# Optimization experiments

Measured on AMD Instinct MI355X. Metric: run time of the kernel, lower is better.

## Reference

```python
import jax, jax.numpy as jnp
import numpy as np
import math

SCALES = (1, 2, 4)
GROUPS = 8
EPS = 1e-5
TEMPERATURE = 1.0


def bilinear_resize(x, out_h, out_w):
    # torch F.interpolate mode='bilinear', align_corners=False
    B, C, h, w = x.shape
    def coords(out, in_):
        c = (jnp.arange(out, dtype=x.dtype) + 0.5) * (in_ / out) - 0.5
        c = jnp.clip(c, 0.0, in_ - 1.0)
        i0 = jnp.floor(c).astype(jnp.int32)
        i1 = jnp.minimum(i0 + 1, in_ - 1)
        t = c - i0.astype(x.dtype)
        return i0, i1, t
    y0, y1, ty = coords(out_h, h)
    x0, x1, tx = coords(out_w, w)
    r0 = x[:, :, y0, :]
    r1 = x[:, :, y1, :]
    v00 = r0[:, :, :, x0]; v01 = r0[:, :, :, x1]
    v10 = r1[:, :, :, x0]; v11 = r1[:, :, :, x1]
    top = v00 * (1.0 - tx) + v01 * tx
    bot = v10 * (1.0 - tx) + v11 * tx
    return top * (1.0 - ty)[:, None] + bot * ty[:, None]


def group_norm(x, gamma, beta):
    B, C, H, W = x.shape
    xg = x.reshape(B, GROUPS, C // GROUPS, H, W)
    mu = xg.mean(axis=(2, 3, 4), keepdims=True)
    var = xg.var(axis=(2, 3, 4), keepdims=True)
    xn = ((xg - mu) * jax.lax.rsqrt(var + EPS)).reshape(B, C, H, W)
    return xn * gamma[None, :, None, None] + beta[None, :, None, None]


def setup_inputs() -> dict:
    key = jax.random.key(0)
    B, C, H, W = 4, 128, 64, 64
    inter = max(C // 4, 8)  # 32
    S = len(SCALES)
    ks = jax.random.split(key, 8)
    def xavier(k, shape, fan_in, fan_out):
        a = math.sqrt(6.0 / (fan_in + fan_out))
        return jax.random.uniform(k, shape, jnp.float32, -a, a)
    inp = {
        'x': jax.random.normal(ks[0], (B, C, H, W), jnp.float32),
        'gn_w': jnp.ones((S, C), jnp.float32),
        'gn_b': jnp.zeros((S, C), jnp.float32),
        'qw': xavier(ks[1], (S, inter, C), C, inter),
        'qb': jnp.zeros((S, inter), jnp.float32),
        'kw': xavier(ks[2], (S, inter, C), C, inter),
        'kb': jnp.zeros((S, inter), jnp.float32),
        'vw': xavier(ks[3], (S, inter, C), C, inter),
        'vb': jnp.zeros((S, inter), jnp.float32),
        'ow': xavier(ks[4], (S, C, inter), inter, C),
        'ob': jnp.zeros((S, C), jnp.float32),
        'gamma': jnp.full((S,), 0.1 / S, jnp.float32),
        'scale_weights': jnp.full((S,), 1.0 / S, jnp.float32),
    }
    return inp


def _forward(x, gn_w, gn_b, qw, qb, kw, kb, vw, vb, ow, ob, gamma, scale_weights):
    B, C, H, W = x.shape
    inter = qw.shape[1]
    inv_scale = 1.0 / (TEMPERATURE * math.sqrt(inter))
    outs = []
    for i, s in enumerate(SCALES):
        if s == 1:
            xs = x
        else:
            xs = x.reshape(B, C, H // s, s, W // s, s).mean(axis=(3, 5))
        h, w = xs.shape[2], xs.shape[3]
        N = h * w
        xn = group_norm(xs, gn_w[i], gn_b[i])
        # 1x1 convs as channel contractions
        q = (jnp.einsum('oc,bchw->bohw', qw[i], xn) + qb[i][None, :, None, None]).reshape(B, inter, N)
        k = (jnp.einsum('oc,bchw->bohw', kw[i], xn) + kb[i][None, :, None, None]).reshape(B, inter, N)
        v = (jnp.einsum('oc,bchw->bohw', vw[i], xn) + vb[i][None, :, None, None]).reshape(B, inter, N)
        logits = jnp.einsum('bin,bim->bnm', q, k) * inv_scale  # [B, N, N]
        attn = jax.nn.softmax(logits, axis=-1)
        att = jnp.einsum('bnm,bim->bin', attn, v).reshape(B, inter, h, w)
        o = jnp.einsum('ci,bihw->bchw', ow[i], att) + ob[i][None, :, None, None]
        y = gamma[i] * o + xs
        if s > 1:
            y = bilinear_resize(y, H, W)
        outs.append(y)
    wts = jax.nn.softmax(scale_weights, axis=0)
    fused = wts[0] * outs[0]
    for i in range(1, len(outs)):
        fused = fused + wts[i] * outs[i]
    return fused


def reference(x, gn_w, gn_b, qw, qb, kw, kb, vw, vb, ow, ob, gamma, scale_weights):
    return _forward(x, gn_w, gn_b, qw, qb, kw, kb, vw, vb, ow, ob, gamma, scale_weights)
```

## Files before the change

kernel.cpp:

```cpp
#include <hip/hip_runtime.h>
#include <math.h>

#define B 4
#define C 128
#define G 8
#define CPG 16
#define INTER 32
#define SPLIT 16
#define KS 4

#define N1 4096
#define N2 1024
#define N4 256

#define QOFF2 (B * N1 * 32)
#define QOFF4 (QOFF2 + B * N2 * 32)
#define QTOT  (QOFF4 + B * N4 * 32)
#define PAOFF2 (B * KS * 32 * N1)
#define PAOFF4 (PAOFF2 + B * KS * 32 * N2)
#define PATOT  (PAOFF4 + B * KS * 32 * N4)
#define PMOFF2 (B * KS * 2 * N1)
#define PMOFF4 (PMOFF2 + B * KS * 2 * N2)
#define PMTOT  (PMOFF4 + B * KS * 2 * N4)

typedef unsigned short ushort_t;
typedef __attribute__((ext_vector_type(8))) short short8;
typedef __attribute__((ext_vector_type(4))) short short4v;
typedef __attribute__((ext_vector_type(4))) float f32x4;

__device__ __forceinline__ ushort_t f2bf(float f) {
    union { float f; unsigned u; } x; x.f = f;
    unsigned r = x.u + 0x7fffu + ((x.u >> 16) & 1u);
    return (ushort_t)(r >> 16);
}

__device__ __forceinline__ void scale_wts(const float* __restrict__ sw,
                                          float& w0, float& w1, float& w2) {
    float a = sw[0], b = sw[1], c = sw[2];
    float m = fmaxf(a, fmaxf(b, c));
    float e0 = __expf(a - m), e1 = __expf(b - m), e2 = __expf(c - m);
    float inv = 1.0f / (e0 + e1 + e2);
    w0 = e0 * inv; w1 = e1 * inv; w2 = e2 * inv;
}

__device__ __forceinline__ void block_reduce_write(float s, float q,
                                                   float* __restrict__ dst2) {
    __shared__ float rs[256], rq[256];
    rs[threadIdx.x] = s; rq[threadIdx.x] = q;
    __syncthreads();
    for (int st = 128; st > 0; st >>= 1) {
        if (threadIdx.x < st) {
            rs[threadIdx.x] += rs[threadIdx.x + st];
            rq[threadIdx.x] += rq[threadIdx.x + st];
        }
        __syncthreads();
    }
    if (threadIdx.x == 0) { dst2[0] = rs[0]; dst2[1] = rq[0]; }
}

__global__ __launch_bounds__(256) void pool_stats_kernel(const float* __restrict__ x,
                                                         float* __restrict__ xs2,
                                                         float* __restrict__ xs4,
                                                         float* __restrict__ part) {
    int bid = blockIdx.x;
    if (bid < 512) {
        int sp = bid & 15, bg = bid >> 4;
        const float* base = x + ((bg * CPG) << 12) + sp * 4096;
        float s = 0.0f, q = 0.0f;
        for (int i = threadIdx.x; i < 4096; i += 256) {
            float v = base[i];
            s += v; q += v * v;
        }
        block_reduce_write(s, q, part + bid * 2);
    } else if (bid < 1024) {
        int blk = bid - 512;
        int sp = blk & 15, bg = blk >> 4;
        int bc = bg * CPG + sp;
        const float* src = x + (bc << 12);
        float* dst = xs2 + (bc << 10);
        float s = 0.0f, q = 0.0f;
        for (int p = threadIdx.x; p < 1024; p += 256) {
            int oy = p >> 5, ox = p & 31;
            const float* s2 = src + oy * 128 + ox * 2;
            float v = (s2[0] + s2[1] + s2[64] + s2[65]) * 0.25f;
            dst[p] = v; s += v; q += v * v;
        }
        block_reduce_write(s, q, part + 1024 + blk * 2);
    } else {
        int blk = bid - 1024;
        int sp = blk & 15, bg = blk >> 4;
        int bc = bg * CPG + sp;
        const float* src = x + (bc << 12);
        float* dst = xs4 + (bc << 8);
        float s = 0.0f, q = 0.0f;
        if (threadIdx.x < 256) {
            int p = threadIdx.x;
            int oy = p >> 4, ox = p & 15;
            const float* s4 = src + oy * 256 + ox * 4;
            float v = 0.0f;
            #pragma unroll
            for (int dy = 0; dy < 4; ++dy)
                #pragma unroll
                for (int dx = 0; dx < 4; ++dx) v += s4[dy * 64 + dx];
            v *= 0.0625f;
            dst[p] = v; s = v; q = v * v;
        }
        block_reduce_write(s, q, part + 2048 + blk * 2);
    }
}

template <int N, int NSH>
__device__ __forceinline__ void qkv_body(int bi, const float* __restrict__ xs,
    const float* __restrict__ part,
    const float* __restrict__ gn_w, const float* __restrict__ gn_b,
    const float* __restrict__ qw, const float* __restrict__ qb,
    const float* __restrict__ kw, const float* __restrict__ kb,
    const float* __restrict__ vw, const float* __restrict__ vb,
    ushort_t* __restrict__ q_bf, ushort_t* __restrict__ k_bf, ushort_t* __restrict__ v_bf) {
    const int nc = N >> 8;
    int nchunk = bi % nc; bi /= nc;
    int og = bi & 3; bi >>= 2;
    int proj = bi % 3; int b = bi / 3;
    const float* wp = (proj == 0) ? qw : ((proj == 1) ? kw : vw);
    const float* bp = (proj == 0) ? qb : ((proj == 1) ? kb : vb);
    __shared__ float wl[8 * 128];
    __shared__ float2 ss[128];
    {
        int t = threadIdx.x;
        #pragma unroll
        for (int r = 0; r < 4; ++r) {
            int e = r * 256 + t;
            int o = e >> 7, c0 = e & 127;
            wl[c0 * 8 + o] = wp[(og * 8 + o) * C + c0];
        }
        if (t < 128) {
            int c = t;
            int bg = b * 8 + (c >> 4);
            float s = 0.0f, q = 0.0f;
            #pragma unroll
            for (int sp = 0; sp < SPLIT; ++sp) {
                s += part[(bg * SPLIT + sp) * 2];
                q += part[(bg * SPLIT + sp) * 2 + 1];
            }
            float inv = 1.0f / (float)(CPG << NSH);
            float mu = s * inv;
            float var = q * inv - mu * mu;
            float rsig = rsqrtf(var + 1e-5f);
            float a = rsig * gn_w[c];
            float2 r; r.x = a; r.y = gn_b[c] - mu * a;
            ss[c] = r;
        }
    }
    __syncthreads();
    int n = nchunk * 256 + threadIdx.x;
    const float* xb = xs + ((size_t)(b * C) << NSH) + n;
    float acc[8];
    #pragma unroll
    for (int o = 0; o < 8; ++o) acc[o] = bp[og * 8 + o];
    #pragma unroll 2
    for (int c0 = 0; c0 < C; ++c0) {
        float raw = xb[(size_t)c0 << NSH];
        float2 s2 = ss[c0];
        float xv = fmaf(s2.x, raw, s2.y);
        const float4* wr = (const float4*)&wl[c0 * 8];
        float4 w0 = wr[0], w1 = wr[1];
        acc[0] += w0.x * xv; acc[1] += w0.y * xv; acc[2] += w0.z * xv; acc[3] += w0.w * xv;
        acc[4] += w1.x * xv; acc[5] += w1.y * xv; acc[6] += w1.z * xv; acc[7] += w1.w * xv;
    }
    if (proj < 2) {
        ushort_t tmp[8];
        #pragma unroll
        for (int o = 0; o < 8; ++o) tmp[o] = f2bf(acc[o]);
        ushort_t* dst = ((proj == 0) ? q_bf : k_bf) + ((size_t)(b * N + n)) * 32 + og * 8;
        *(uint4*)dst = *(const uint4*)tmp;
    } else {
        #pragma unroll
        for (int o = 0; o < 8; ++o)
            v_bf[((size_t)(b * 32 + og * 8 + o) << NSH) + n] = f2bf(acc[o]);
    }
}

__global__ __launch_bounds__(256) void qkv_all_kernel(const float* __restrict__ x,
    const float* __restrict__ xs2, const float* __restrict__ xs4,
    const float* __restrict__ part,
    const float* __restrict__ gn_w, const float* __restrict__ gn_b,
    const float* __restrict__ qw, const float* __restrict__ qb,
    const float* __restrict__ kw, const float* __restrict__ kb,
    const float* __restrict__ vw, const float* __restrict__ vb,
    ushort_t* __restrict__ qbf, ushort_t* __restrict__ kbf, ushort_t* __restrict__ vbf) {
    int bid = blockIdx.x;
    if (bid < 768) {
        qkv_body<N1, 12>(bid, x, part, gn_w, gn_b, qw, qb, kw, kb, vw, vb, qbf, kbf, vbf);
    } else if (bid < 960) {
        qkv_body<N2, 10>(bid - 768, xs2, part + 1024, gn_w + C, gn_b + C,
                         qw + INTER * C, qb + INTER, kw + INTER * C, kb + INTER,
                         vw + INTER * C, vb + INTER,
                         qbf + QOFF2, kbf + QOFF2, vbf + QOFF2);
    } else {
        qkv_body<N4, 8>(bid - 960, xs4, part + 2048, gn_w + 2 * C, gn_b + 2 * C,
                        qw + 2 * INTER * C, qb + 2 * INTER, kw + 2 * INTER * C, kb + 2 * INTER,
                        vw + 2 * INTER * C, vb + 2 * INTER,
                        qbf + QOFF4, kbf + QOFF4, vbf + QOFF4);
    }
}

template <int N, int NSH>
__device__ __forceinline__ void attn_body(int bi,
    const ushort_t* __restrict__ q_bf, const ushort_t* __restrict__ k_bf,
    const ushort_t* __restrict__ v_bf,
    float* __restrict__ pacc, float* __restrict__ pml,
    ushort_t* K_lds, ushort_t* V_lds, ushort_t* P_lds) {
    int ks = bi % KS; bi /= KS;
    const int nqc = N >> 6;
    int qc = bi % nqc; int b = bi / nqc;
    int tid = threadIdx.x;
    int l = tid & 63, w = tid >> 6, lq = l & 15, g = l >> 4;
    int q0 = qc * 64 + w * 16;
    const float invs = 0.17677669529663687f;

    short8 qf = *(const short8*)(q_bf + ((size_t)(b * N + q0 + lq)) * 32 + g * 8);
    f32x4 acco0 = {0.f, 0.f, 0.f, 0.f}, acco1 = {0.f, 0.f, 0.f, 0.f};
    float mrun = -3.0e38f, lrun = 0.0f;

    const int kchunk = N / KS;
    int kbase = ks * kchunk;
    const int ntiles = kchunk >> 6;
    ushort_t* Pw = P_lds + w * 16 * 72;

    for (int t = 0; t < ntiles; ++t) {
        int kt0 = kbase + t * 64;
        __syncthreads();
        {
            const uint4* ksrc = (const uint4*)(k_bf + ((size_t)(b * N + kt0 + (tid >> 2))) * 32 + (tid & 3) * 8);
            *(uint4*)&K_lds[(tid >> 2) * 40 + (tid & 3) * 8] = *ksrc;
            const uint4* vsrc = (const uint4*)(v_bf + (((size_t)(b * 32 + (tid >> 3))) << NSH) + kt0 + (tid & 7) * 8);
            *(uint4*)&V_lds[(tid >> 3) * 72 + (tid & 7) * 8] = *vsrc;
        }
        __syncthreads();

        f32x4 sa[4];
        #pragma unroll
        for (int kt = 0; kt < 4; ++kt) {
            short8 kf = *(const short8*)&K_lds[(kt * 16 + lq) * 40 + g * 8];
            f32x4 z = {0.f, 0.f, 0.f, 0.f};
            sa[kt] = __builtin_amdgcn_mfma_f32_16x16x32_bf16(kf, qf, z, 0, 0, 0);
        }
        float sc[16];
        #pragma unroll
        for (int kt = 0; kt < 4; ++kt) {
            sc[kt * 4 + 0] = sa[kt][0] * invs;
            sc[kt * 4 + 1] = sa[kt][1] * invs;
            sc[kt * 4 + 2] = sa[kt][2] * invs;
            sc[kt * 4 + 3] = sa[kt][3] * invs;
        }
        float tmax = sc[0];
        #pragma unroll
        for (int j = 1; j < 16; ++j) tmax = fmaxf(tmax, sc[j]);
        tmax = fmaxf(tmax, __shfl_xor(tmax, 16, 64));
        tmax = fmaxf(tmax, __shfl_xor(tmax, 32, 64));
        float nm = fmaxf(mrun, tmax);
        float corr = __expf(mrun - nm);
        float psum = 0.0f;
        ushort_t pb[16];
        #pragma unroll
        for (int j = 0; j < 16; ++j) {
            float p = __expf(sc[j] - nm);
            psum += p;
            pb[j] = f2bf(p);
        }
        psum += __shfl_xor(psum, 16, 64);
        psum += __shfl_xor(psum, 32, 64);
        lrun = lrun * corr + psum;
        mrun = nm;
        #pragma unroll
        for (int e = 0; e < 4; ++e) { acco0[e] *= corr; acco1[e] *= corr; }
        #pragma unroll
        for (int kt = 0; kt < 4; ++kt) {
            short4v pv4;
            pv4[0] = (short)pb[kt * 4 + 0];
            pv4[1] = (short)pb[kt * 4 + 1];
            pv4[2] = (short)pb[kt * 4 + 2];
            pv4[3] = (short)pb[kt * 4 + 3];
            *(short4v*)&Pw[lq * 72 + kt * 16 + g * 4] = pv4;
        }
        #pragma unroll
        for (int c = 0; c < 2; ++c) {
            short8 pf  = *(const short8*)&Pw[lq * 72 + c * 32 + g * 8];
            short8 vf0 = *(const short8*)&V_lds[(lq) * 72 + c * 32 + g * 8];
            short8 vf1 = *(const short8*)&V_lds[(16 + lq) * 72 + c * 32 + g * 8];
            acco0 = __builtin_amdgcn_mfma_f32_16x16x32_bf16(vf0, pf, acco0, 0, 0, 0);
            acco1 = __builtin_amdgcn_mfma_f32_16x16x32_bf16(vf1, pf, acco1, 0, 0, 0);
        }
    }
    int n = q0 + lq;
    size_t pb_ = ((size_t)(b * KS + ks)) * 32;
    #pragma unroll
    for (int r = 0; r < 4; ++r) {
        pacc[(pb_ + (g * 4 + r)) * N + n]      = acco0[r];
        pacc[(pb_ + 16 + (g * 4 + r)) * N + n] = acco1[r];
    }
    if (g == 0) {
        pml[((size_t)(b * KS + ks) * 2) * N + n]     = mrun;
        pml[((size_t)(b * KS + ks) * 2 + 1) * N + n] = lrun;
    }
}

__global__ __launch_bounds__(256) void attn_all_kernel(
    const ushort_t* __restrict__ qbf, const ushort_t* __restrict__ kbf,
    const ushort_t* __restrict__ vbf,
    float* __restrict__ pacc, float* __restrict__ pml) {
    __shared__ ushort_t K_lds[64 * 40];
    __shared__ ushort_t V_lds[32 * 72];
    __shared__ ushort_t P_lds[4 * 16 * 72];
    int bid = blockIdx.x;
    if (bid < 1024) {
        attn_body<N1, 12>(bid, qbf, kbf, vbf, pacc, pml, K_lds, V_lds, P_lds);
    } else if (bid < 1280) {
        attn_body<N2, 10>(bid - 1024, qbf + QOFF2, kbf + QOFF2, vbf + QOFF2,
                          pacc + PAOFF2, pml + PMOFF2, K_lds, V_lds, P_lds);
    } else {
        attn_body<N4, 8>(bid - 1280, qbf + QOFF4, kbf + QOFF4, vbf + QOFF4,
                         pacc + PAOFF4, pml + PMOFF4, K_lds, V_lds, P_lds);
    }
}

template <int N, int NSH>
__device__ __forceinline__ void comb_oy_body(int tile, const float* __restrict__ pacc,
                                             const float* __restrict__ pml,
                                             const float* __restrict__ ow,
                                             const float* __restrict__ ob,
                                             const float* __restrict__ gamma,
                                             const float* __restrict__ xs,
                                             float* __restrict__ ydst,
                                             const float* __restrict__ sw,
                                             float* att_lds, float* ow_lds) {
    const int ntiles = N >> 5;
    int b = tile / ntiles;
    int n0 = (tile % ntiles) << 5;
    int t = threadIdx.x;
    {
        const float4* src = (const float4*)ow;
        float4* dst = (float4*)ow_lds;
        dst[t] = src[t];
        dst[256 + t] = src[256 + t];
        dst[512 + t] = src[512 + t];
        dst[768 + t] = src[768 + t];
    }
    {
        int o = t >> 3, j = t & 3, half = (t >> 2) & 1;
        o = t >> 3; j = t & 7;
        int n = n0 + j * 4;
        float4 mv[KS], lv[KS], av[KS];
        float4 M = {-3.0e38f, -3.0e38f, -3.0e38f, -3.0e38f};
        #pragma unroll
        for (int ks = 0; ks < KS; ++ks) {
            mv[ks] = *(const float4*)&pml[((size_t)(b * KS + ks) * 2) * N + n];
            lv[ks] = *(const float4*)&pml[((size_t)(b * KS + ks) * 2 + 1) * N + n];
            av[ks] = *(const float4*)&pacc[((size_t)(b * KS + ks) * INTER + o) * N + n];
            M.x = fmaxf(M.x, mv[ks].x); M.y = fmaxf(M.y, mv[ks].y);
            M.z = fmaxf(M.z, mv[ks].z); M.w = fmaxf(M.w, mv[ks].w);
        }
        float4 L = {0.f, 0.f, 0.f, 0.f}, A = {0.f, 0.f, 0.f, 0.f};
        #pragma unroll
        for (int ks = 0; ks < KS; ++ks) {
            float4 wgt;
            wgt.x = __expf(mv[ks].x - M.x); wgt.y = __expf(mv[ks].y - M.y);
            wgt.z = __expf(mv[ks].z - M.z); wgt.w = __expf(mv[ks].w - M.w);
            L.x += lv[ks].x * wgt.x; L.y += lv[ks].y * wgt.y;
            L.z += lv[ks].z * wgt.z; L.w += lv[ks].w * wgt.w;
            A.x += av[ks].x * wgt.x; A.y += av[ks].y * wgt.y;
            A.z += av[ks].z * wgt.z; A.w += av[ks].w * wgt.w;
        }
        float4 r;
        r.x = A.x / L.x; r.y = A.y / L.y; r.z = A.z / L.z; r.w = A.w / L.w;
        *(float4*)&att_lds[o * 36 + j * 4] = r;
    }
    __syncthreads();
    {
        int n = t & 31;
        int cg = t >> 5;
        float av[INTER];
        #pragma unroll
        for (int i = 0; i < INTER; ++i) av[i] = att_lds[i * 36 + n];
        float gm = gamma[0];
        float wsc = 1.0f;
        bool scale = (sw != nullptr);
        if (scale) { float w0, w1, w2; scale_wts(sw, w0, w1, w2); wsc = w0; }
        const float* xsb = xs + ((size_t)(b * C + cg * 16) << NSH) + n0 + n;
        float* yb = ydst + ((size_t)(b * C + cg * 16) << NSH) + n0 + n;
        #pragma unroll
        for (int cc = 0; cc < 16; ++cc) {
            int c = cg * 16 + cc;
            const float4* wr = (const float4*)&ow_lds[c * 32];
            float a0 = 0.f, a1 = 0.f, a2 = 0.f, a3 = 0.f;
            #pragma unroll
            for (int i4 = 0; i4 < 8; ++i4) {
                float4 wv = wr[i4];
                a0 += wv.x * av[i4 * 4 + 0];
                a1 += wv.y * av[i4 * 4 + 1];
                a2 += wv.z * av[i4 * 4 + 2];
                a3 += wv.w * av[i4 * 4 + 3];
            }
            float o = ob[c] + ((a0 + a1) + (a2 + a3));
            float y = gm * o + xsb[(size_t)cc << NSH];
            yb[(size_t)cc << NSH] = wsc * y;
        }
    }
}

__global__ __launch_bounds__(256) void comb_oy_all_kernel(const float* __restrict__ pacc,
    const float* __restrict__ pml,
    const float* __restrict__ ow, const float* __restrict__ ob,
    const float* __restrict__ gamma,
    const float* __restrict__ x, const float* __restrict__ xs2, const float* __restrict__ xs4,
    float* __restrict__ out, float* __restrict__ y2, float* __restrict__ y4,
    const float* __restrict__ sw) {
    __shared__ float att_lds[32 * 36];
    __shared__ float ow_lds[128 * 32];
    int bid = blockIdx.x;
    if (bid < 512) {
        comb_oy_body<N1, 12>(bid, pacc, pml, ow, ob, gamma, x, out, sw, att_lds, ow_lds);
    } else if (bid < 640) {
        comb_oy_body<N2, 10>(bid - 512, pacc + PAOFF2, pml + PMOFF2,
                             ow + C * INTER, ob + C, gamma + 1, xs2, y2, nullptr,
                             att_lds, ow_lds);
    } else {
        comb_oy_body<N4, 8>(bid - 640, pacc + PAOFF4, pml + PMOFF4,
                            ow + 2 * C * INTER, ob + 2 * C, gamma + 2, xs4, y4, nullptr,
                            att_lds, ow_lds);
    }
}

__device__ __forceinline__ float bilerp(const float* __restrict__ img, int in,
                                        int oy, int ox, float r) {
    float cy = (oy + 0.5f) * r - 0.5f;
    cy = fminf(fmaxf(cy, 0.0f), (float)(in - 1));
    float cx = (ox + 0.5f) * r - 0.5f;
    cx = fminf(fmaxf(cx, 0.0f), (float)(in - 1));
    int y0 = (int)cy; int y1i = (y0 + 1 < in) ? y0 + 1 : in - 1; float ty = cy - (float)y0;
    int x0 = (int)cx; int x1i = (x0 + 1 < in) ? x0 + 1 : in - 1; float tx = cx - (float)x0;
    float v00 = img[y0 * in + x0];
    float v01 = img[y0 * in + x1i];
    float v10 = img[y1i * in + x0];
    float v11 = img[y1i * in + x1i];
    float top = v00 * (1.0f - tx) + v01 * tx;
    float bot = v10 * (1.0f - tx) + v11 * tx;
    return top * (1.0f - ty) + bot * ty;
}

__global__ __launch_bounds__(256) void fuse_kernel(float* __restrict__ out,
                                                   const float* __restrict__ y2,
                                                   const float* __restrict__ y4,
                                                   const float* __restrict__ sw) {
    int idx = blockIdx.x * 256 + threadIdx.x;
    int p = idx & 4095;
    int bc = idx >> 12;
    int oy = p >> 6, ox = p & 63;
    float w0, w1, w2; scale_wts(sw, w0, w1, w2);
    float v2 = bilerp(y2 + bc * 1024, 32, oy, ox, 0.5f);
    float v4 = bilerp(y4 + bc * 256, 16, oy, ox, 0.25f);
    out[idx] = out[idx] + w1 * v2 + w2 * v4;
}

extern "C" void kernel_launch(void* const* d_in, const int* in_sizes, int n_in,
                              void* d_out, int out_size, void* d_ws, size_t ws_size,
                              hipStream_t stream) {
    const float* x     = (const float*)d_in[0];
    const float* gn_w  = (const float*)d_in[1];
    const float* gn_b  = (const float*)d_in[2];
    const float* qw    = (const float*)d_in[3];
    const float* qb    = (const float*)d_in[4];
    const float* kw    = (const float*)d_in[5];
    const float* kb    = (const float*)d_in[6];
    const float* vw    = (const float*)d_in[7];
    const float* vb    = (const float*)d_in[8];
    const float* ow    = (const float*)d_in[9];
    const float* ob    = (const float*)d_in[10];
    const float* gamma = (const float*)d_in[11];
    const float* sw    = (const float*)d_in[12];
    float* out = (float*)d_out;

    float* ws    = (float*)d_ws;
    float* xs2   = ws;
    float* xs4   = xs2 + 524288;
    float* y2    = xs4 + 131072;
    float* y4    = y2 + 524288;
    float* part  = y4 + 131072;
    float* pacc  = part + 3072;
    float* pml   = pacc + PATOT;
    ushort_t* qbf = (ushort_t*)(pml + PMTOT);
    ushort_t* kbf = qbf + QTOT;
    ushort_t* vbf = kbf + QTOT;

    pool_stats_kernel<<<1536, 256, 0, stream>>>(x, xs2, xs4, part);
    qkv_all_kernel<<<1008, 256, 0, stream>>>(x, xs2, xs4, part, gn_w, gn_b,
                                             qw, qb, kw, kb, vw, vb, qbf, kbf, vbf);
    attn_all_kernel<<<1344, 256, 0, stream>>>(qbf, kbf, vbf, pacc, pml);
    comb_oy_all_kernel<<<672, 256, 0, stream>>>(pacc, pml, ow, ob, gamma,
                                                x, xs2, xs4, out, y2, y4, sw);
    fuse_kernel<<<8192, 256, 0, stream>>>(out, y2, y4, sw);
}
```

Measured before the change: 81.76 us.

## Fuse small-scale attention with output projection and merge scale-1 combine with fusion

Scales 2 and 4 now run attention over the full key range in one block, skipping the key split, and apply the output projection and residual directly. This removes their partial-accumulator round trip. The scale-1 combine kernel now also does the bilinear upsampling and weighted sum of y2/y4, which removes the separate fuse kernel launch and an extra pass over the output. Softmax uses exp2 with a log2e-folded scale. The trade-off is less parallelism for the small scales, with 64-key-tile serial loops per block, and the combine kernel gathers y2/y4 per channel.

```diff
diff --git a/kernel.cpp b/kernel.cpp
--- a/kernel.cpp
+++ b/kernel.cpp
@@ -3,7 +3,6 @@
 
 #define B 4
 #define C 128
-#define G 8
 #define CPG 16
 #define INTER 32
 #define SPLIT 16
@@ -16,12 +15,8 @@
 #define QOFF2 (B * N1 * 32)
 #define QOFF4 (QOFF2 + B * N2 * 32)
 #define QTOT  (QOFF4 + B * N4 * 32)
-#define PAOFF2 (B * KS * 32 * N1)
-#define PAOFF4 (PAOFF2 + B * KS * 32 * N2)
-#define PATOT  (PAOFF4 + B * KS * 32 * N4)
-#define PMOFF2 (B * KS * 2 * N1)
-#define PMOFF4 (PMOFF2 + B * KS * 2 * N2)
-#define PMTOT  (PMOFF4 + B * KS * 2 * N4)
+#define PATOT (B * KS * 32 * N1)
+#define PMTOT (B * KS * 2 * N1)
 
 typedef unsigned short ushort_t;
 typedef __attribute__((ext_vector_type(8))) short short8;
@@ -92,20 +87,17 @@
         int bc = bg * CPG + sp;
         const float* src = x + (bc << 12);
         float* dst = xs4 + (bc << 8);
-        float s = 0.0f, q = 0.0f;
-        if (threadIdx.x < 256) {
-            int p = threadIdx.x;
-            int oy = p >> 4, ox = p & 15;
-            const float* s4 = src + oy * 256 + ox * 4;
-            float v = 0.0f;
+        int p = threadIdx.x & 255;
+        int oy = p >> 4, ox = p & 15;
+        const float* s4 = src + oy * 256 + ox * 4;
+        float v = 0.0f;
+        #pragma unroll
+        for (int dy = 0; dy < 4; ++dy)
             #pragma unroll
-            for (int dy = 0; dy < 4; ++dy)
-                #pragma unroll
-                for (int dx = 0; dx < 4; ++dx) v += s4[dy * 64 + dx];
-            v *= 0.0625f;
-            dst[p] = v; s = v; q = v * v;
-        }
-        block_reduce_write(s, q, part + 2048 + blk * 2);
+            for (int dx = 0; dx < 4; ++dx) v += s4[dy * 64 + dx];
+        v *= 0.0625f;
+        dst[p] = v;
+        block_reduce_write(v, v * v, part + 2048 + blk * 2);
     }
 }
 
@@ -145,8 +137,7 @@
             float inv = 1.0f / (float)(CPG << NSH);
             float mu = s * inv;
             float var = q * inv - mu * mu;
-            float rsig = rsqrtf(var + 1e-5f);
-            float a = rsig * gn_w[c];
+            float a = rsqrtf(var + 1e-5f) * gn_w[c];
             float2 r; r.x = a; r.y = gn_b[c] - mu * a;
             ss[c] = r;
         }
@@ -204,6 +195,71 @@
     }
 }
 
+#define ATTN_TILE_STEP(kt0)                                                                   \
+    {                                                                                         \
+        __syncthreads();                                                                      \
+        const uint4* ksrc = (const uint4*)(k_bf + ((size_t)(b * N + (kt0) + (tid >> 2))) * 32 \
+                                           + (tid & 3) * 8);                                  \
+        *(uint4*)&K_lds[(tid >> 2) * 40 + (tid & 3) * 8] = *ksrc;                             \
+        const uint4* vsrc = (const uint4*)(v_bf + (((size_t)(b * 32 + (tid >> 3))) << NSH)    \
+                                           + (kt0) + (tid & 7) * 8);                          \
+        *(uint4*)&V_lds[(tid >> 3) * 72 + (tid & 7) * 8] = *vsrc;                             \
+        __syncthreads();                                                                      \
+        f32x4 sa[4];                                                                          \
+        _Pragma("unroll")                                                                     \
+        for (int kt = 0; kt < 4; ++kt) {                                                      \
+            short8 kf = *(const short8*)&K_lds[(kt * 16 + lq) * 40 + g * 8];                  \
+            f32x4 z = {0.f, 0.f, 0.f, 0.f};                                                   \
+            sa[kt] = __builtin_amdgcn_mfma_f32_16x16x32_bf16(kf, qf, z, 0, 0, 0);             \
+        }                                                                                     \
+        float sc[16];                                                                         \
+        _Pragma("unroll")                                                                     \
+        for (int kt = 0; kt < 4; ++kt) {                                                      \
+            sc[kt * 4 + 0] = sa[kt][0] * invs;                                                \
+            sc[kt * 4 + 1] = sa[kt][1] * invs;                                                \
+            sc[kt * 4 + 2] = sa[kt][2] * invs;                                                \
+            sc[kt * 4 + 3] = sa[kt][3] * invs;                                                \
+        }                                                                                     \
+        float tmax = sc[0];                                                                   \
+        _Pragma("unroll")                                                                     \
+        for (int j = 1; j < 16; ++j) tmax = fmaxf(tmax, sc[j]);                               \
+        tmax = fmaxf(tmax, __shfl_xor(tmax, 16, 64));                                         \
+        tmax = fmaxf(tmax, __shfl_xor(tmax, 32, 64));                                         \
+        float nm = fmaxf(mrun, tmax);                                                         \
+        float corr = exp2f(mrun - nm);                                                        \
+        float psum = 0.0f;                                                                    \
+        ushort_t pb[16];                                                                      \
+        _Pragma("unroll")                                                                     \
+        for (int j = 0; j < 16; ++j) {                                                        \
+            float p = exp2f(sc[j] - nm);                                                      \
+            psum += p;                                                                        \
+            pb[j] = f2bf(p);                                                                  \
+        }                                                                                     \
+        psum += __shfl_xor(psum, 16, 64);                                                     \
+        psum += __shfl_xor(psum, 32, 64);                                                     \
+        lrun = lrun * corr + psum;                                                            \
+        mrun = nm;                                                                            \
+        _Pragma("unroll")                                                                     \
+        for (int e = 0; e < 4; ++e) { acco0[e] *= corr; acco1[e] *= corr; }                   \
+        _Pragma("unroll")                                                                     \
+        for (int kt = 0; kt < 4; ++kt) {                                                      \
+            short4v pv4;                                                                      \
+            pv4[0] = (short)pb[kt * 4 + 0];                                                   \
+            pv4[1] = (short)pb[kt * 4 + 1];                                                   \
+            pv4[2] = (short)pb[kt * 4 + 2];                                                   \
+            pv4[3] = (short)pb[kt * 4 + 3];                                                   \
+            *(short4v*)&Pw[lq * 72 + kt * 16 + g * 4] = pv4;                                  \
+        }                                                                                     \
+        _Pragma("unroll")                                                                     \
+        for (int c = 0; c < 2; ++c) {                                                         \
+            short8 pf  = *(const short8*)&Pw[lq * 72 + c * 32 + g * 8];                       \
+            short8 vf0 = *(const short8*)&V_lds[(lq) * 72 + c * 32 + g * 8];                  \
+            short8 vf1 = *(const short8*)&V_lds[(16 + lq) * 72 + c * 32 + g * 8];             \
+            acco0 = __builtin_amdgcn_mfma_f32_16x16x32_bf16(vf0, pf, acco0, 0, 0, 0);         \
+            acco1 = __builtin_amdgcn_mfma_f32_16x16x32_bf16(vf1, pf, acco1, 0, 0, 0);         \
+        }                                                                                     \
+    }
+
 template <int N, int NSH>
 __device__ __forceinline__ void attn_body(int bi,
     const ushort_t* __restrict__ q_bf, const ushort_t* __restrict__ k_bf,
@@ -216,7 +272,7 @@
     int tid = threadIdx.x;
     int l = tid & 63, w = tid >> 6, lq = l & 15, g = l >> 4;
     int q0 = qc * 64 + w * 16;
-    const float invs = 0.17677669529663687f;
+    const float invs = 0.17677669529663687f * 1.4426950408889634f;
 
     short8 qf = *(const short8*)(q_bf + ((size_t)(b * N + q0 + lq)) * 32 + g * 8);
     f32x4 acco0 = {0.f, 0.f, 0.f, 0.f}, acco1 = {0.f, 0.f, 0.f, 0.f};
@@ -224,73 +280,11 @@
 
     const int kchunk = N / KS;
     int kbase = ks * kchunk;
-    const int ntiles = kchunk >> 6;
     ushort_t* Pw = P_lds + w * 16 * 72;
 
-    for (int t = 0; t < ntiles; ++t) {
+    for (int t = 0; t < (kchunk >> 6); ++t) {
         int kt0 = kbase + t * 64;
-        __syncthreads();
-        {
-            const uint4* ksrc = (const uint4*)(k_bf + ((size_t)(b * N + kt0 + (tid >> 2))) * 32 + (tid & 3) * 8);
-            *(uint4*)&K_lds[(tid >> 2) * 40 + (tid & 3) * 8] = *ksrc;
-            const uint4* vsrc = (const uint4*)(v_bf + (((size_t)(b * 32 + (tid >> 3))) << NSH) + kt0 + (tid & 7) * 8);
-            *(uint4*)&V_lds[(tid >> 3) * 72 + (tid & 7) * 8] = *vsrc;
-        }
-        __syncthreads();
-
-        f32x4 sa[4];
-        #pragma unroll
-        for (int kt = 0; kt < 4; ++kt) {
-            short8 kf = *(const short8*)&K_lds[(kt * 16 + lq) * 40 + g * 8];
-            f32x4 z = {0.f, 0.f, 0.f, 0.f};
-            sa[kt] = __builtin_amdgcn_mfma_f32_16x16x32_bf16(kf, qf, z, 0, 0, 0);
-        }
-        float sc[16];
-        #pragma unroll
-        for (int kt = 0; kt < 4; ++kt) {
-            sc[kt * 4 + 0] = sa[kt][0] * invs;
-            sc[kt * 4 + 1] = sa[kt][1] * invs;
-            sc[kt * 4 + 2] = sa[kt][2] * invs;
-            sc[kt * 4 + 3] = sa[kt][3] * invs;
-        }
-        float tmax = sc[0];
-        #pragma unroll
-        for (int j = 1; j < 16; ++j) tmax = fmaxf(tmax, sc[j]);
-        tmax = fmaxf(tmax, __shfl_xor(tmax, 16, 64));
-        tmax = fmaxf(tmax, __shfl_xor(tmax, 32, 64));
-        float nm = fmaxf(mrun, tmax);
-        float corr = __expf(mrun - nm);
-        float psum = 0.0f;
-        ushort_t pb[16];
-        #pragma unroll
-        for (int j = 0; j < 16; ++j) {
-            float p = __expf(sc[j] - nm);
-            psum += p;
-            pb[j] = f2bf(p);
-        }
-        psum += __shfl_xor(psum, 16, 64);
-        psum += __shfl_xor(psum, 32, 64);
-        lrun = lrun * corr + psum;
-        mrun = nm;
-        #pragma unroll
-        for (int e = 0; e < 4; ++e) { acco0[e] *= corr; acco1[e] *= corr; }
-        #pragma unroll
-        for (int kt = 0; kt < 4; ++kt) {
-            short4v pv4;
-            pv4[0] = (short)pb[kt * 4 + 0];
-            pv4[1] = (short)pb[kt * 4 + 1];
-            pv4[2] = (short)pb[kt * 4 + 2];
-            pv4[3] = (short)pb[kt * 4 + 3];
-            *(short4v*)&Pw[lq * 72 + kt * 16 + g * 4] = pv4;
-        }
-        #pragma unroll
-        for (int c = 0; c < 2; ++c) {
-            short8 pf  = *(const short8*)&Pw[lq * 72 + c * 32 + g * 8];
-            short8 vf0 = *(const short8*)&V_lds[(lq) * 72 + c * 32 + g * 8];
-            short8 vf1 = *(const short8*)&V_lds[(16 + lq) * 72 + c * 32 + g * 8];
-            acco0 = __builtin_amdgcn_mfma_f32_16x16x32_bf16(vf0, pf, acco0, 0, 0, 0);
-            acco1 = __builtin_amdgcn_mfma_f32_16x16x32_bf16(vf1, pf, acco1, 0, 0, 0);
-        }
+        ATTN_TILE_STEP(kt0)
     }
     int n = q0 + lq;
     size_t pb_ = ((size_t)(b * KS + ks)) * 32;
@@ -305,71 +299,133 @@
     }
 }
 
+template <int N, int NSH>
+__device__ __forceinline__ void attn_oy_body(int bi,
+    const ushort_t* __restrict__ q_bf, const ushort_t* __restrict__ k_bf,
+    const ushort_t* __restrict__ v_bf,
+    const float* __restrict__ ow, const float* __restrict__ ob,
+    const float* __restrict__ gamma,
+    const float* __restrict__ xs, float* __restrict__ ydst,
+    ushort_t* K_lds, ushort_t* V_lds, ushort_t* P_lds) {
+    const int nqc = N >> 6;
+    int qc = bi % nqc; int b = bi / nqc;
+    int tid = threadIdx.x;
+    int l = tid & 63, w = tid >> 6, lq = l & 15, g = l >> 4;
+    int q0 = qc * 64 + w * 16;
+    const float invs = 0.17677669529663687f * 1.4426950408889634f;
+
+    short8 qf = *(const short8*)(q_bf + ((size_t)(b * N + q0 + lq)) * 32 + g * 8);
+    f32x4 acco0 = {0.f, 0.f, 0.f, 0.f}, acco1 = {0.f, 0.f, 0.f, 0.f};
+    float mrun = -3.0e38f, lrun = 0.0f;
+    ushort_t* Pw = P_lds + w * 16 * 72;
+
+    for (int t = 0; t < (N >> 6); ++t) {
+        int kt0 = t * 64;
+        ATTN_TILE_STEP(kt0)
+    }
+    __syncthreads();
+    float* att_lds = (float*)P_lds;
+    float invl = 1.0f / lrun;
+    #pragma unroll
+    for (int r = 0; r < 4; ++r) {
+        att_lds[(g * 4 + r) * 66 + w * 16 + lq]      = acco0[r] * invl;
+        att_lds[(16 + g * 4 + r) * 66 + w * 16 + lq] = acco1[r] * invl;
+    }
+    __syncthreads();
+    {
+        int n = tid & 63;
+        int cg = tid >> 6;
+        int nb = qc * 64;
+        float av[32];
+        #pragma unroll
+        for (int i = 0; i < 32; ++i) av[i] = att_lds[i * 66 + n];
+        float gm = gamma[0];
+        const float* xsb = xs + ((size_t)(b * C + cg * 32) << NSH) + nb + n;
+        float* yb = ydst + ((size_t)(b * C + cg * 32) << NSH) + nb + n;
+        #pragma unroll 4
+        for (int cc = 0; cc < 32; ++cc) {
+            int c = cg * 32 + cc;
+            const float4* wr = (const float4*)&ow[c * 32];
+            float a0 = 0.f, a1 = 0.f, a2 = 0.f, a3 = 0.f;
+            #pragma unroll
+            for (int i4 = 0; i4 < 8; ++i4) {
+                float4 wv = wr[i4];
+                a0 += wv.x * av[i4 * 4 + 0]; a1 += wv.y * av[i4 * 4 + 1];
+                a2 += wv.z * av[i4 * 4 + 2]; a3 += wv.w * av[i4 * 4 + 3];
+            }
+            float o_ = ob[c] + ((a0 + a1) + (a2 + a3));
+            yb[(size_t)cc << NSH] = gm * o_ + xsb[(size_t)cc << NSH];
+        }
+    }
+}
+
 __global__ __launch_bounds__(256) void attn_all_kernel(
     const ushort_t* __restrict__ qbf, const ushort_t* __restrict__ kbf,
     const ushort_t* __restrict__ vbf,
-    float* __restrict__ pacc, float* __restrict__ pml) {
+    float* __restrict__ pacc, float* __restrict__ pml,
+    const float* __restrict__ ow, const float* __restrict__ ob,
+    const float* __restrict__ gamma,
+    const float* __restrict__ xs2, const float* __restrict__ xs4,
+    float* __restrict__ y2, float* __restrict__ y4) {
     __shared__ ushort_t K_lds[64 * 40];
     __shared__ ushort_t V_lds[32 * 72];
     __shared__ ushort_t P_lds[4 * 16 * 72];
     int bid = blockIdx.x;
     if (bid < 1024) {
         attn_body<N1, 12>(bid, qbf, kbf, vbf, pacc, pml, K_lds, V_lds, P_lds);
-    } else if (bid < 1280) {
-        attn_body<N2, 10>(bid - 1024, qbf + QOFF2, kbf + QOFF2, vbf + QOFF2,
-                          pacc + PAOFF2, pml + PMOFF2, K_lds, V_lds, P_lds);
+    } else if (bid < 1088) {
+        attn_oy_body<N2, 10>(bid - 1024, qbf + QOFF2, kbf + QOFF2, vbf + QOFF2,
+                             ow + C * INTER, ob + C, gamma + 1, xs2, y2,
+                             K_lds, V_lds, P_lds);
     } else {
-        attn_body<N4, 8>(bid - 1280, qbf + QOFF4, kbf + QOFF4, vbf + QOFF4,
-                         pacc + PAOFF4, pml + PMOFF4, K_lds, V_lds, P_lds);
-    }
-}
-
-template <int N, int NSH>
-__device__ __forceinline__ void comb_oy_body(int tile, const float* __restrict__ pacc,
-                                             const float* __restrict__ pml,
-                                             const float* __restrict__ ow,
-                                             const float* __restrict__ ob,
-                                             const float* __restrict__ gamma,
-                                             const float* __restrict__ xs,
-                                             float* __restrict__ ydst,
-                                             const float* __restrict__ sw,
-                                             float* att_lds, float* ow_lds) {
-    const int ntiles = N >> 5;
-    int b = tile / ntiles;
-    int n0 = (tile % ntiles) << 5;
+        attn_oy_body<N4, 8>(bid - 1088, qbf + QOFF4, kbf + QOFF4, vbf + QOFF4,
+                            ow + 2 * C * INTER, ob + 2 * C, gamma + 2, xs4, y4,
+                            K_lds, V_lds, P_lds);
+    }
+}
+
+__global__ __launch_bounds__(256) void comb_oy_s1_fuse_kernel(
+    const float* __restrict__ pacc, const float* __restrict__ pml,
+    const float* __restrict__ ow, const float* __restrict__ ob,
+    const float* __restrict__ gamma, const float* __restrict__ x,
+    const float* __restrict__ y2, const float* __restrict__ y4,
+    float* __restrict__ out, const float* __restrict__ sw) {
+    __shared__ float att_lds[32 * 36];
+    __shared__ float ow_lds[128 * 32];
+    const int N = N1;
+    int tile = blockIdx.x;
+    int b = tile >> 7;
+    int n0 = (tile & 127) << 5;
     int t = threadIdx.x;
     {
         const float4* src = (const float4*)ow;
         float4* dst = (float4*)ow_lds;
-        dst[t] = src[t];
-        dst[256 + t] = src[256 + t];
-        dst[512 + t] = src[512 + t];
-        dst[768 + t] = src[768 + t];
+        dst[t] = src[t]; dst[256 + t] = src[256 + t];
+        dst[512 + t] = src[512 + t]; dst[768 + t] = src[768 + t];
     }
     {
-        int o = t >> 3, j = t & 3, half = (t >> 2) & 1;
-        o = t >> 3; j = t & 7;
+        int o = t >> 3, j = t & 7;
         int n = n0 + j * 4;
-        float4 mv[KS], lv[KS], av[KS];
+        float4 mv[KS], lv[KS], av4[KS];
         float4 M = {-3.0e38f, -3.0e38f, -3.0e38f, -3.0e38f};
         #pragma unroll
-        for (int ks = 0; ks < KS; ++ks) {
-            mv[ks] = *(const float4*)&pml[((size_t)(b * KS + ks) * 2) * N + n];
-            lv[ks] = *(const float4*)&pml[((size_t)(b * KS + ks) * 2 + 1) * N + n];
-            av[ks] = *(const float4*)&pacc[((size_t)(b * KS + ks) * INTER + o) * N + n];
-            M.x = fmaxf(M.x, mv[ks].x); M.y = fmaxf(M.y, mv[ks].y);
-            M.z = fmaxf(M.z, mv[ks].z); M.w = fmaxf(M.w, mv[ks].w);
+        for (int k2 = 0; k2 < KS; ++k2) {
+            mv[k2]  = *(const float4*)&pml[((size_t)(b * KS + k2) * 2) * N + n];
+            lv[k2]  = *(const float4*)&pml[((size_t)(b * KS + k2) * 2 + 1) * N + n];
+            av4[k2] = *(const float4*)&pacc[((size_t)(b * KS + k2) * INTER + o) * N + n];
+            M.x = fmaxf(M.x, mv[k2].x); M.y = fmaxf(M.y, mv[k2].y);
+            M.z = fmaxf(M.z, mv[k2].z); M.w = fmaxf(M.w, mv[k2].w);
         }
         float4 L = {0.f, 0.f, 0.f, 0.f}, A = {0.f, 0.f, 0.f, 0.f};
         #pragma unroll
-        for (int ks = 0; ks < KS; ++ks) {
-            float4 wgt;
-            wgt.x = __expf(mv[ks].x - M.x); wgt.y = __expf(mv[ks].y - M.y);
-            wgt.z = __expf(mv[ks].z - M.z); wgt.w = __expf(mv[ks].w - M.w);
-            L.x += lv[ks].x * wgt.x; L.y += lv[ks].y * wgt.y;
-            L.z += lv[ks].z * wgt.z; L.w += lv[ks].w * wgt.w;
-            A.x += av[ks].x * wgt.x; A.y += av[ks].y * wgt.y;
-            A.z += av[ks].z * wgt.z; A.w += av[ks].w * wgt.w;
+        for (int k2 = 0; k2 < KS; ++k2) {
+            float4 wg;
+            wg.x = exp2f(mv[k2].x - M.x); wg.y = exp2f(mv[k2].y - M.y);
+            wg.z = exp2f(mv[k2].z - M.z); wg.w = exp2f(mv[k2].w - M.w);
+            L.x += lv[k2].x * wg.x; L.y += lv[k2].y * wg.y;
+            L.z += lv[k2].z * wg.z; L.w += lv[k2].w * wg.w;
+            A.x += av4[k2].x * wg.x; A.y += av4[k2].y * wg.y;
+            A.z += av4[k2].z * wg.z; A.w += av4[k2].w * wg.w;
         }
         float4 r;
         r.x = A.x / L.x; r.y = A.y / L.y; r.z = A.z / L.z; r.w = A.w / L.w;
@@ -377,89 +433,49 @@
     }
     __syncthreads();
     {
-        int n = t & 31;
-        int cg = t >> 5;
-        float av[INTER];
-        #pragma unroll
-        for (int i = 0; i < INTER; ++i) av[i] = att_lds[i * 36 + n];
+        int n = t & 31, cg2 = t >> 5;
+        float av[32];
+        #pragma unroll
+        for (int i = 0; i < 32; ++i) av[i] = att_lds[i * 36 + n];
         float gm = gamma[0];
-        float wsc = 1.0f;
-        bool scale = (sw != nullptr);
-        if (scale) { float w0, w1, w2; scale_wts(sw, w0, w1, w2); wsc = w0; }
-        const float* xsb = xs + ((size_t)(b * C + cg * 16) << NSH) + n0 + n;
-        float* yb = ydst + ((size_t)(b * C + cg * 16) << NSH) + n0 + n;
-        #pragma unroll
+        float w0, w1, w2; scale_wts(sw, w0, w1, w2);
+        int p = n0 + n, oy = p >> 6, ox = p & 63;
+        float cy2 = fminf(fmaxf((oy + 0.5f) * 0.5f - 0.5f, 0.0f), 31.0f);
+        int ya0 = (int)cy2; int ya1 = (ya0 + 1 < 32) ? ya0 + 1 : 31; float ty2 = cy2 - (float)ya0;
+        float cx2 = fminf(fmaxf((ox + 0.5f) * 0.5f - 0.5f, 0.0f), 31.0f);
+        int xa0 = (int)cx2; int xa1 = (xa0 + 1 < 32) ? xa0 + 1 : 31; float tx2 = cx2 - (float)xa0;
+        float cy4 = fminf(fmaxf((oy + 0.5f) * 0.25f - 0.5f, 0.0f), 15.0f);
+        int yb0 = (int)cy4; int yb1 = (yb0 + 1 < 16) ? yb0 + 1 : 15; float ty4 = cy4 - (float)yb0;
+        float cx4 = fminf(fmaxf((ox + 0.5f) * 0.25f - 0.5f, 0.0f), 15.0f);
+        int xb0 = (int)cx4; int xb1 = (xb0 + 1 < 16) ? xb0 + 1 : 15; float tx4 = cx4 - (float)xb0;
+        const float* xsb = x + ((size_t)(b * C + cg2 * 16) << 12) + p;
+        float* outp = out + ((size_t)(b * C + cg2 * 16) << 12) + p;
+        const float* y2b = y2 + (size_t)(b * C + cg2 * 16) * 1024;
+        const float* y4b = y4 + (size_t)(b * C + cg2 * 16) * 256;
+        #pragma unroll 4
         for (int cc = 0; cc < 16; ++cc) {
-            int c = cg * 16 + cc;
+            int c = cg2 * 16 + cc;
             const float4* wr = (const float4*)&ow_lds[c * 32];
             float a0 = 0.f, a1 = 0.f, a2 = 0.f, a3 = 0.f;
             #pragma unroll
             for (int i4 = 0; i4 < 8; ++i4) {
                 float4 wv = wr[i4];
-                a0 += wv.x * av[i4 * 4 + 0];
-                a1 += wv.y * av[i4 * 4 + 1];
-                a2 += wv.z * av[i4 * 4 + 2];
-                a3 += wv.w * av[i4 * 4 + 3];
+                a0 += wv.x * av[i4 * 4 + 0]; a1 += wv.y * av[i4 * 4 + 1];
+                a2 += wv.z * av[i4 * 4 + 2]; a3 += wv.w * av[i4 * 4 + 3];
             }
-            float o = ob[c] + ((a0 + a1) + (a2 + a3));
-            float y = gm * o + xsb[(size_t)cc << NSH];
-            yb[(size_t)cc << NSH] = wsc * y;
-        }
-    }
-}
-
-__global__ __launch_bounds__(256) void comb_oy_all_kernel(const float* __restrict__ pacc,
-    const float* __restrict__ pml,
-    const float* __restrict__ ow, const float* __restrict__ ob,
-    const float* __restrict__ gamma,
-    const float* __restrict__ x, const float* __restrict__ xs2, const float* __restrict__ xs4,
-    float* __restrict__ out, float* __restrict__ y2, float* __restrict__ y4,
-    const float* __restrict__ sw) {
-    __shared__ float att_lds[32 * 36];
-    __shared__ float ow_lds[128 * 32];
-    int bid = blockIdx.x;
-    if (bid < 512) {
-        comb_oy_body<N1, 12>(bid, pacc, pml, ow, ob, gamma, x, out, sw, att_lds, ow_lds);
-    } else if (bid < 640) {
-        comb_oy_body<N2, 10>(bid - 512, pacc + PAOFF2, pml + PMOFF2,
-                             ow + C * INTER, ob + C, gamma + 1, xs2, y2, nullptr,
-                             att_lds, ow_lds);
-    } else {
-        comb_oy_body<N4, 8>(bid - 640, pacc + PAOFF4, pml + PMOFF4,
-                            ow + 2 * C * INTER, ob + 2 * C, gamma + 2, xs4, y4, nullptr,
-                            att_lds, ow_lds);
-    }
-}
-
-__device__ __forceinline__ float bilerp(const float* __restrict__ img, int in,
-                                        int oy, int ox, float r) {
-    float cy = (oy + 0.5f) * r - 0.5f;
-    cy = fminf(fmaxf(cy, 0.0f), (float)(in - 1));
-    float cx = (ox + 0.5f) * r - 0.5f;
-    cx = fminf(fmaxf(cx, 0.0f), (float)(in - 1));
-    int y0 = (int)cy; int y1i = (y0 + 1 < in) ? y0 + 1 : in - 1; float ty = cy - (float)y0;
-    int x0 = (int)cx; int x1i = (x0 + 1 < in) ? x0 + 1 : in - 1; float tx = cx - (float)x0;
-    float v00 = img[y0 * in + x0];
-    float v01 = img[y0 * in + x1i];
-    float v10 = img[y1i * in + x0];
-    float v11 = img[y1i * in + x1i];
-    float top = v00 * (1.0f - tx) + v01 * tx;
-    float bot = v10 * (1.0f - tx) + v11 * tx;
-    return top * (1.0f - ty) + bot * ty;
-}
-
-__global__ __launch_bounds__(256) void fuse_kernel(float* __restrict__ out,
-                                                   const float* __restrict__ y2,
-                                                   const float* __restrict__ y4,
-                                                   const float* __restrict__ sw) {
-    int idx = blockIdx.x * 256 + threadIdx.x;
-    int p = idx & 4095;
-    int bc = idx >> 12;
-    int oy = p >> 6, ox = p & 63;
-    float w0, w1, w2; scale_wts(sw, w0, w1, w2);
-    float v2 = bilerp(y2 + bc * 1024, 32, oy, ox, 0.5f);
-    float v4 = bilerp(y4 + bc * 256, 16, oy, ox, 0.25f);
-    out[idx] = out[idx] + w1 * v2 + w2 * v4;
+            float o_ = ob[c] + ((a0 + a1) + (a2 + a3));
+            float yv = gm * o_ + xsb[(size_t)cc << 12];
+            const float* i2 = y2b + cc * 1024;
+            float top2 = i2[ya0 * 32 + xa0] * (1.f - tx2) + i2[ya0 * 32 + xa1] * tx2;
+            float bot2 = i2[ya1 * 32 + xa0] * (1.f - tx2) + i2[ya1 * 32 + xa1] * tx2;
+            float v2 = top2 * (1.f - ty2) + bot2 * ty2;
+            const float* i4p = y4b + cc * 256;
+            float top4 = i4p[yb0 * 16 + xb0] * (1.f - tx4) + i4p[yb0 * 16 + xb1] * tx4;
+            float bot4 = i4p[yb1 * 16 + xb0] * (1.f - tx4) + i4p[yb1 * 16 + xb1] * tx4;
+            float v4 = top4 * (1.f - ty4) + bot4 * ty4;
+            outp[(size_t)cc << 12] = w0 * yv + w1 * v2 + w2 * v4;
+        }
+    }
 }
 
 extern "C" void kernel_launch(void* const* d_in, const int* in_sizes, int n_in,
@@ -495,8 +511,8 @@
     pool_stats_kernel<<<1536, 256, 0, stream>>>(x, xs2, xs4, part);
     qkv_all_kernel<<<1008, 256, 0, stream>>>(x, xs2, xs4, part, gn_w, gn_b,
                                              qw, qb, kw, kb, vw, vb, qbf, kbf, vbf);
-    attn_all_kernel<<<1344, 256, 0, stream>>>(qbf, kbf, vbf, pacc, pml);
-    comb_oy_all_kernel<<<672, 256, 0, stream>>>(pacc, pml, ow, ob, gamma,
-                                                x, xs2, xs4, out, y2, y4, sw);
-    fuse_kernel<<<8192, 256, 0, stream>>>(out, y2, y4, sw);
-}
+    attn_all_kernel<<<1104, 256, 0, stream>>>(qbf, kbf, vbf, pacc, pml,
+                                              ow, ob, gamma, xs2, xs4, y2, y4);
+    comb_oy_s1_fuse_kernel<<<512, 256, 0, stream>>>(pacc, pml, ow, ob, gamma,
+                                                    x, y2, y4, out, sw);
+}
```

Result: slower. 117.0 us (+43.2%).
